# Optimization experiments

Hardware: AMD Instinct MI355X
Metric: run time of the kernel (lower is better)

## Reference

```python
import jax, jax.numpy as jnp
import numpy as np

B, T, S, E, D = 16, 1024, 1024, 1024, 1024  # batch, trg_len, src_len, enc_dim, trg_dim

def setup_inputs() -> dict:
    key = jax.random.key(0)
    k1, k2, k3, k4, k5 = jax.random.split(key, 5)
    sc = 0.02
    return {
        "hidden": jax.random.normal(k1, (B, T, D), dtype=jnp.float32),
        "encoder_outputs": jax.random.normal(k2, (B, S, E), dtype=jnp.float32),
        "W_attn": jax.random.normal(k3, (D, E), dtype=jnp.float32) * sc,
        "b_attn": jax.random.normal(k4, (D,), dtype=jnp.float32) * sc,
        "W_out": jax.random.normal(k5, (D, E + D), dtype=jnp.float32) * sc,
    }

def reference(hidden, encoder_outputs, W_attn, b_attn, W_out):
    # score, method='general': energies = Linear(enc_out) ; bmm(hidden, energies^T)
    proj = jnp.einsum('bse,de->bsd', encoder_outputs, W_attn) + b_attn  # (B,S,D)
    attn_energies = jnp.einsum('btd,bsd->bts', hidden, proj)            # (B,T,S)
    attn_weights = jax.nn.softmax(attn_energies, axis=-1)               # (B,T,S)
    weighted_context = jnp.einsum('bts,bse->bte', attn_weights, encoder_outputs)  # (B,T,E)
    h_cat = jnp.concatenate([weighted_context, hidden], axis=-1)        # (B,T,E+D)
    h_tilde = jnp.tanh(jnp.einsum('btc,dc->btd', h_cat, W_out))         # (B,T,D)
    return h_tilde, attn_weights, attn_energies
```

## Files before the change

### kernel.cpp

```cpp
#include <hip/hip_runtime.h>
#include <stdint.h>


typedef __bf16 bf16x8 __attribute__((ext_vector_type(8)));
typedef float  f32x4  __attribute__((ext_vector_type(4)));

enum { MODE_PROJ = 0, MODE_ENERGY = 1, MODE_WC = 2, MODE_OUT = 3 };

__device__ __forceinline__ ushort f2bf(float f) {
    uint32_t u = __builtin_bit_cast(uint32_t, f);
    u += 0x7fffu + ((u >> 16) & 1u);
    return (ushort)(u >> 16);
}

#define GLB_PTR(p) ((const __attribute__((address_space(1))) void*)(p))
#define LDS_PTR(p) ((__attribute__((address_space(3))) void*)(p))

__device__ __forceinline__ void stage_tile(const ushort* __restrict__ g, int ld,
                                           ushort* lds, int wave, int lane) {
#pragma unroll
    for (int i = 0; i < 4; ++i) {
        const int seg  = i * 8 + wave;
        const int p    = seg * 1024 + lane * 16;
        const int row  = p >> 7;
        const int cpos = (p >> 4) & 7;
        const int csrc = cpos ^ (row & 7);
        const ushort* gp = g + (size_t)row * ld + csrc * 8;
        __builtin_amdgcn_global_load_lds(GLB_PTR(gp), LDS_PTR((char*)lds + seg * 1024), 16, 0, 0);
    }
}

template <int MODE>
__global__ __launch_bounds__(512, 2) void gemm_bt(
    const ushort* __restrict__ A0, const ushort* __restrict__ A1,
    const ushort* __restrict__ B0, const float* __restrict__ bias,
    ushort* __restrict__ out_bf, float* __restrict__ out_f)
{
    constexpr int    KTOT   = (MODE == MODE_OUT) ? 2048 : 1024;
    constexpr int    LDB    = (MODE == MODE_OUT) ? 2048 : 1024;
    constexpr int    NT     = KTOT / 64;
    constexpr size_t BBATCH = (MODE == MODE_ENERGY || MODE == MODE_WC) ? ((size_t)1 << 20) : 0;

    const int flat = (blockIdx.z * 4 + blockIdx.y) * 4 + blockIdx.x;
    const int nid  = ((flat & 7) << 5) | (flat >> 3);
    const int b    = nid >> 4;
    const int bm   = ((nid >> 2) & 3) << 8;
    const int bn   = (nid & 3) << 8;

    const int wave = threadIdx.x >> 6;
    const int lane = threadIdx.x & 63;
    const int wm   = wave >> 2;
    const int wn   = wave & 3;

    const ushort* Ab0 = A0 + ((size_t)b << 20) + (size_t)bm * 1024;
    const ushort* Ab1 = nullptr;
    if constexpr (MODE == MODE_OUT) Ab1 = A1 + ((size_t)b << 20) + (size_t)bm * 1024;
    const ushort* Bb0 = B0 + (size_t)b * BBATCH + (size_t)bn * LDB;

    __shared__ ushort ldsA[2][256 * 64];
    __shared__ ushort ldsB[2][256 * 64];

    f32x4 acc[8][4];
#pragma unroll
    for (int r = 0; r < 8; ++r)
#pragma unroll
        for (int c = 0; c < 4; ++c) acc[r][c] = f32x4{0.f, 0.f, 0.f, 0.f};

    auto stage_step = [&](int t, int buf) {
        const int k0 = t * 64;
        const ushort* Ag; int kA;
        if constexpr (MODE == MODE_OUT) { Ag = (k0 < 1024) ? Ab0 : Ab1; kA = k0 & 1023; }
        else                            { Ag = Ab0;                     kA = k0; }
        stage_tile(Ag + kA, 1024, ldsA[buf], wave, lane);
        stage_tile(Bb0 + k0, LDB,  ldsB[buf], wave, lane);
    };

    auto compute_step = [&](int buf) {
#pragma unroll
        for (int ks = 0; ks < 2; ++ks) {
            const int quad = lane >> 4;
            const int l15  = lane & 15;
            const int chunk = ks * 4 + quad;
            bf16x8 af[8], bfr[4];
#pragma unroll
            for (int r = 0; r < 8; ++r) {
                const int row = wm * 128 + r * 16 + l15;
                af[r] = *(const bf16x8*)&ldsA[buf][row * 64 + ((chunk ^ (row & 7)) * 8)];
            }
#pragma unroll
            for (int c = 0; c < 4; ++c) {
                const int row = wn * 64 + c * 16 + l15;
                bfr[c] = *(const bf16x8*)&ldsB[buf][row * 64 + ((chunk ^ (row & 7)) * 8)];
            }
            __builtin_amdgcn_s_setprio(1);
#pragma unroll
            for (int r = 0; r < 8; ++r)
#pragma unroll
                for (int c = 0; c < 4; ++c)
                    acc[r][c] = __builtin_amdgcn_mfma_f32_16x16x32_bf16(af[r], bfr[c], acc[r][c], 0, 0, 0);
            __builtin_amdgcn_s_setprio(0);
        }
    };

    stage_step(0, 0);
    __syncthreads();

    for (int t = 0; t < NT; t += 2) {
        stage_step(t + 1, 1);
        compute_step(0);
        __syncthreads();
        if (t + 2 < NT) stage_step(t + 2, 0);
        compute_step(1);
        __syncthreads();
    }

    const size_t obase = (size_t)b << 20;
    const int quad = lane >> 4;
    const int l15  = lane & 15;
#pragma unroll
    for (int r = 0; r < 8; ++r) {
#pragma unroll
        for (int c = 0; c < 4; ++c) {
#pragma unroll
            for (int g = 0; g < 4; ++g) {
                const int row = bm + wm * 128 + r * 16 + quad * 4 + g;
                const int col = bn + wn * 64 + c * 16 + l15;
                float v = acc[r][c][g];
                const size_t idx = obase + (size_t)row * 1024 + col;
                if constexpr (MODE == MODE_PROJ) {
                    out_bf[idx] = f2bf(v + bias[col]);
                } else if constexpr (MODE == MODE_ENERGY) {
                    out_f[idx] = v;
                } else if constexpr (MODE == MODE_WC) {
                    out_bf[idx] = f2bf(v);
                } else {
                    out_f[idx] = tanhf(v);
                }
            }
        }
    }
}

__global__ __launch_bounds__(256) void conv_k(const float* __restrict__ in,
                                              ushort* __restrict__ out) {
    const size_t i = (size_t)blockIdx.x * 256 + threadIdx.x;
    float4 v = ((const float4*)in)[i];
    ushort4 o;
    o.x = f2bf(v.x); o.y = f2bf(v.y); o.z = f2bf(v.z); o.w = f2bf(v.w);
    ((ushort4*)out)[i] = o;
}

__global__ __launch_bounds__(256) void transconv_k(const float* __restrict__ in,
                                                   ushort* __restrict__ outT,
                                                   ushort* __restrict__ outN) {
    __shared__ ushort t[64][65];
    const int b  = blockIdx.z;
    const int s0 = blockIdx.y * 64, e0 = blockIdx.x * 64;
    const float* ip = in   + ((size_t)b << 20);
    ushort*      tp = outT + ((size_t)b << 20);
    ushort*      np = outN + ((size_t)b << 20);
    const int tx = threadIdx.x & 15;
    const int ty = threadIdx.x >> 4;
#pragma unroll
    for (int i = 0; i < 4; ++i) {
        const int s = ty + i * 16;
        float4 v = *(const float4*)&ip[(size_t)(s0 + s) * 1024 + e0 + tx * 4];
        ushort4 n4;
        n4.x = f2bf(v.x); n4.y = f2bf(v.y); n4.z = f2bf(v.z); n4.w = f2bf(v.w);
        *(ushort4*)&np[(size_t)(s0 + s) * 1024 + e0 + tx * 4] = n4;
        t[tx * 4 + 0][s] = n4.x; t[tx * 4 + 1][s] = n4.y;
        t[tx * 4 + 2][s] = n4.z; t[tx * 4 + 3][s] = n4.w;
    }
    __syncthreads();
#pragma unroll
    for (int i = 0; i < 4; ++i) {
        const int e = ty + i * 16;
        ushort4 v;
        v.x = t[e][tx * 4 + 0]; v.y = t[e][tx * 4 + 1];
        v.z = t[e][tx * 4 + 2]; v.w = t[e][tx * 4 + 3];
        *(ushort4*)&tp[(size_t)(e0 + e) * 1024 + s0 + tx * 4] = v;
    }
}

__global__ __launch_bounds__(256) void softmax_k(const float* __restrict__ en,
                                                 float* __restrict__ w,
                                                 ushort* __restrict__ wbf) {
    const size_t row = blockIdx.x;
    const float* e = en + (row << 10);
    const int tid = threadIdx.x;
    const int wv = tid >> 6, ln = tid & 63;

    float4 v = ((const float4*)e)[tid];
    float m = fmaxf(fmaxf(v.x, v.y), fmaxf(v.z, v.w));
#pragma unroll
    for (int o = 32; o; o >>= 1) m = fmaxf(m, __shfl_xor(m, o, 64));
    __shared__ float sm[4];
    if (!ln) sm[wv] = m;
    __syncthreads();
    m = fmaxf(fmaxf(sm[0], sm[1]), fmaxf(sm[2], sm[3]));

    const float e0 = expf(v.x - m), e1 = expf(v.y - m), e2 = expf(v.z - m), e3 = expf(v.w - m);
    float s = e0 + e1 + e2 + e3;
#pragma unroll
    for (int o = 32; o; o >>= 1) s += __shfl_xor(s, o, 64);
    __shared__ float ss[4];
    if (!ln) ss[wv] = s;
    __syncthreads();
    s = ss[0] + ss[1] + ss[2] + ss[3];
    const float inv = 1.0f / s;

    const float w0 = e0 * inv, w1 = e1 * inv, w2 = e2 * inv, w3 = e3 * inv;
    ((float4*)(w + (row << 10)))[tid] = float4{w0, w1, w2, w3};
    ushort4 o4;
    o4.x = f2bf(w0); o4.y = f2bf(w1); o4.z = f2bf(w2); o4.w = f2bf(w3);
    ((ushort4*)(wbf + (row << 10)))[tid] = o4;
}

extern "C" void kernel_launch(void* const* d_in, const int* in_sizes, int n_in,
                              void* d_out, int out_size, void* d_ws, size_t ws_size,
                              hipStream_t stream) {
    (void)in_sizes; (void)n_in; (void)out_size; (void)ws_size;
    const float* hidden = (const float*)d_in[0];
    const float* enc    = (const float*)d_in[1];
    const float* Wattn  = (const float*)d_in[2];
    const float* battn  = (const float*)d_in[3];
    const float* Wout   = (const float*)d_in[4];

    const size_t M16 = (size_t)16 * 1024 * 1024;
    float* out_h = (float*)d_out;
    float* out_w = out_h + M16;
    float* out_e = out_w + M16;

    ushort* ws = (ushort*)d_ws;
    ushort* hidden_bf = ws;
    ushort* encwc_bf  = ws + M16;
    ushort* proj_bf   = ws + 2 * M16;
    ushort* wattn_bf  = ws + 3 * M16;
    ushort* wout_bf   = ws + 3 * M16 + (1u << 20);
    ushort* encT_bf   = (ushort*)out_h;
    ushort* weights_bf = (ushort*)out_h + M16;

    dim3 blkG(512, 1, 1);
    dim3 blk(256, 1, 1);
    dim3 gG(4, 4, 16);
    dim3 gT(16, 16, 16);

    conv_k<<<dim3(16384), blk, 0, stream>>>(hidden, hidden_bf);
    conv_k<<<dim3(1024),  blk, 0, stream>>>(Wattn, wattn_bf);
    conv_k<<<dim3(2048),  blk, 0, stream>>>(Wout, wout_bf);
    transconv_k<<<gT, blk, 0, stream>>>(enc, encT_bf, encwc_bf);
    gemm_bt<MODE_PROJ><<<gG, blkG, 0, stream>>>(encwc_bf, nullptr, wattn_bf, battn,
                                                proj_bf, nullptr);
    gemm_bt<MODE_ENERGY><<<gG, blkG, 0, stream>>>(hidden_bf, nullptr, proj_bf, nullptr,
                                                  nullptr, out_e);
    softmax_k<<<dim3(16 * 1024), blk, 0, stream>>>(out_e, out_w, weights_bf);
    gemm_bt<MODE_WC><<<gG, blkG, 0, stream>>>(weights_bf, nullptr, encT_bf, nullptr,
                                              encwc_bf, nullptr);
    gemm_bt<MODE_OUT><<<gG, blkG, 0, stream>>>(encwc_bf, hidden_bf, wout_bf, nullptr,
                                               nullptr, out_h);
}
```

Baseline: 599.5 us.

## Split GEMM main loop into eight barrier-synced phases with interleaved half-tile loads

Restructures the bf16 MFMA GEMM mainloop so each 64-wide K tile is processed in four quarter phases. Each phase issues a half-tile global-to-LDS load, loads B fragments once per tile and A fragments per quarter, then runs its MFMAs between raw s_barriers. Explicit vmcnt waits replace the __syncthreads-based double buffering. The goal is finer-grained overlap of memory traffic with MFMA work and fewer full waits. The cost is many more barriers, and correctness depends on the hand-tuned vmcnt counts.

```diff
diff --git a/kernel.cpp b/kernel.cpp
--- a/kernel.cpp
+++ b/kernel.cpp
@@ -6,6 +6,8 @@
 typedef float  f32x4  __attribute__((ext_vector_type(4)));
 
 enum { MODE_PROJ = 0, MODE_ENERGY = 1, MODE_WC = 2, MODE_OUT = 3 };
+
+template <int V> struct ic { static constexpr int value = V; };
 
 __device__ __forceinline__ ushort f2bf(float f) {
     uint32_t u = __builtin_bit_cast(uint32_t, f);
@@ -15,11 +17,12 @@
 
 #define GLB_PTR(p) ((const __attribute__((address_space(1))) void*)(p))
 #define LDS_PTR(p) ((__attribute__((address_space(3))) void*)(p))
-
-__device__ __forceinline__ void stage_tile(const ushort* __restrict__ g, int ld,
+#define VMW(N) asm volatile("s_waitcnt vmcnt(" #N ")" ::: "memory")
+
+__device__ __forceinline__ void stage_half(const ushort* __restrict__ g, int ld,
                                            ushort* lds, int wave, int lane) {
 #pragma unroll
-    for (int i = 0; i < 4; ++i) {
+    for (int i = 0; i < 2; ++i) {
         const int seg  = i * 8 + wave;
         const int p    = seg * 1024 + lane * 16;
         const int row  = p >> 7;
@@ -39,6 +42,7 @@
     constexpr int    KTOT   = (MODE == MODE_OUT) ? 2048 : 1024;
     constexpr int    LDB    = (MODE == MODE_OUT) ? 2048 : 1024;
     constexpr int    NT     = KTOT / 64;
+    constexpr int    NITER  = NT / 2;
     constexpr size_t BBATCH = (MODE == MODE_ENERGY || MODE == MODE_WC) ? ((size_t)1 << 20) : 0;
 
     const int flat = (blockIdx.z * 4 + blockIdx.y) * 4 + blockIdx.x;
@@ -66,52 +70,89 @@
 #pragma unroll
         for (int c = 0; c < 4; ++c) acc[r][c] = f32x4{0.f, 0.f, 0.f, 0.f};
 
-    auto stage_step = [&](int t, int buf) {
+    bf16x8 bq[4][2];
+
+    auto stageA = [&](int t, int buf, int h) {
         const int k0 = t * 64;
         const ushort* Ag; int kA;
         if constexpr (MODE == MODE_OUT) { Ag = (k0 < 1024) ? Ab0 : Ab1; kA = k0 & 1023; }
         else                            { Ag = Ab0;                     kA = k0; }
-        stage_tile(Ag + kA, 1024, ldsA[buf], wave, lane);
-        stage_tile(Bb0 + k0, LDB,  ldsB[buf], wave, lane);
+        stage_half(Ag + (size_t)(h * 128) * 1024 + kA, 1024,
+                   &ldsA[buf][h * 128 * 64], wave, lane);
     };
-
-    auto compute_step = [&](int buf) {
-#pragma unroll
-        for (int ks = 0; ks < 2; ++ks) {
-            const int quad = lane >> 4;
-            const int l15  = lane & 15;
-            const int chunk = ks * 4 + quad;
-            bf16x8 af[8], bfr[4];
-#pragma unroll
-            for (int r = 0; r < 8; ++r) {
-                const int row = wm * 128 + r * 16 + l15;
-                af[r] = *(const bf16x8*)&ldsA[buf][row * 64 + ((chunk ^ (row & 7)) * 8)];
+    auto stageB = [&](int t, int buf, int h) {
+        stage_half(Bb0 + (size_t)(h * 128) * LDB + t * 64, LDB,
+                   &ldsB[buf][h * 128 * 64], wave, lane);
+    };
+
+    auto phase = [&](auto BUF, auto Q, auto LB, int wmode) {
+        constexpr int  buf   = decltype(BUF)::value;
+        constexpr int  q     = decltype(Q)::value;
+        constexpr bool loadB = decltype(LB)::value != 0;
+        const int l15  = lane & 15;
+        const int quad = lane >> 4;
+        if constexpr (loadB) {
+#pragma unroll
+            for (int c = 0; c < 4; ++c)
+#pragma unroll
+                for (int ks = 0; ks < 2; ++ks) {
+                    const int row   = wn * 64 + c * 16 + l15;
+                    const int chunk = ks * 4 + quad;
+                    bq[c][ks] = *(const bf16x8*)&ldsB[buf][row * 64 + ((chunk ^ (row & 7)) * 8)];
+                }
+        }
+        bf16x8 aq[2][2];
+#pragma unroll
+        for (int r = 0; r < 2; ++r)
+#pragma unroll
+            for (int ks = 0; ks < 2; ++ks) {
+                const int row   = wm * 128 + (q * 2 + r) * 16 + l15;
+                const int chunk = ks * 4 + quad;
+                aq[r][ks] = *(const bf16x8*)&ldsA[buf][row * 64 + ((chunk ^ (row & 7)) * 8)];
             }
-#pragma unroll
-            for (int c = 0; c < 4; ++c) {
-                const int row = wn * 64 + c * 16 + l15;
-                bfr[c] = *(const bf16x8*)&ldsB[buf][row * 64 + ((chunk ^ (row & 7)) * 8)];
-            }
-            __builtin_amdgcn_s_setprio(1);
-#pragma unroll
-            for (int r = 0; r < 8; ++r)
-#pragma unroll
-                for (int c = 0; c < 4; ++c)
-                    acc[r][c] = __builtin_amdgcn_mfma_f32_16x16x32_bf16(af[r], bfr[c], acc[r][c], 0, 0, 0);
-            __builtin_amdgcn_s_setprio(0);
-        }
+        __builtin_amdgcn_s_barrier();
+        __builtin_amdgcn_s_setprio(1);
+#pragma unroll
+        for (int r = 0; r < 2; ++r)
+#pragma unroll
+            for (int c = 0; c < 4; ++c)
+#pragma unroll
+                for (int ks = 0; ks < 2; ++ks)
+                    acc[q * 2 + r][c] = __builtin_amdgcn_mfma_f32_16x16x32_bf16(
+                        aq[r][ks], bq[c][ks], acc[q * 2 + r][c], 0, 0, 0);
+        __builtin_amdgcn_s_setprio(0);
+        if (wmode == 1)      { VMW(4); }
+        else if (wmode == 2) { VMW(0); }
+        __builtin_amdgcn_s_barrier();
+        __builtin_amdgcn_sched_barrier(0);
     };
 
-    stage_step(0, 0);
-    __syncthreads();
-
-    for (int t = 0; t < NT; t += 2) {
-        stage_step(t + 1, 1);
-        compute_step(0);
-        __syncthreads();
-        if (t + 2 < NT) stage_step(t + 2, 0);
-        compute_step(1);
-        __syncthreads();
+    stageB(0, 0, 0); stageB(0, 0, 1);
+    stageA(0, 0, 0); stageA(0, 0, 1);
+    stageB(1, 1, 0); stageB(1, 1, 1);
+    VMW(4);
+    __builtin_amdgcn_s_barrier();
+    __builtin_amdgcn_sched_barrier(0);
+
+    for (int it = 0; it < NITER; ++it) {
+        const int  tp   = 2 * it;
+        const bool last = (it == NITER - 1);
+        stageA(tp + 1, 1, 0);
+        phase(ic<0>{}, ic<0>{}, ic<1>{}, 0);
+        stageA(tp + 1, 1, 1);
+        phase(ic<0>{}, ic<1>{}, ic<0>{}, 0);
+        if (!last) stageB(tp + 2, 0, 0);
+        phase(ic<0>{}, ic<2>{}, ic<0>{}, 0);
+        if (!last) stageB(tp + 2, 0, 1);
+        phase(ic<0>{}, ic<3>{}, ic<0>{}, last ? 2 : 1);
+        if (!last) stageA(tp + 2, 0, 0);
+        phase(ic<1>{}, ic<0>{}, ic<1>{}, 0);
+        if (!last) stageA(tp + 2, 0, 1);
+        phase(ic<1>{}, ic<1>{}, ic<0>{}, 0);
+        if (!last) stageB(tp + 3, 1, 0);
+        phase(ic<1>{}, ic<2>{}, ic<0>{}, 0);
+        if (!last) stageB(tp + 3, 1, 1);
+        phase(ic<1>{}, ic<3>{}, ic<0>{}, last ? 0 : 1);
     }
 
     const size_t obase = (size_t)b << 20;
```

New measurement: 608.5 us. Within noise of the previous version (+1.5%).
